# Optimization experiments

Measured on AMD Instinct MI355X. Metric: run time of the kernel, lower is better.

Reference implementation:

```python
import jax, jax.numpy as jnp
import numpy as np

B, S, D = 4, 1024, 1024      # batch, seq, dim
H = 1024                     # moe_inter_dim
E = 16                       # n_routed_experts
K = 2                        # n_activated_experts (top-k)
N_IN = 2                     # experts that consume x instead of embeddings
NSH = 2                      # n_shared_experts


def setup_inputs() -> dict:
    key = jax.random.key(0)
    ks = jax.random.split(key, 10)
    s = 0.02
    return {
        "embeddings": jax.random.normal(ks[0], (B, S, D), dtype=jnp.float32),
        "x": jax.random.normal(ks[1], (B * S, D), dtype=jnp.float32),
        "gate_w": jax.random.normal(ks[2], (E, D), dtype=jnp.float32) * s,
        "W1": jax.random.normal(ks[3], (E, D, H), dtype=jnp.float32) * s,
        "B1": jnp.zeros((E, H), dtype=jnp.float32),
        "W2": jax.random.normal(ks[4], (E, H, D), dtype=jnp.float32) * s,
        "B2": jnp.zeros((E, D), dtype=jnp.float32),
        "W3": jax.random.normal(ks[5], (E, D, H), dtype=jnp.float32) * s,
        "B3": jnp.zeros((E, H), dtype=jnp.float32),
        "sW1": jax.random.normal(ks[6], (D, NSH * H), dtype=jnp.float32) * s,
        "sB1": jnp.zeros((NSH * H,), dtype=jnp.float32),
        "sW2": jax.random.normal(ks[7], (NSH * H, D), dtype=jnp.float32) * s,
        "sB2": jnp.zeros((D,), dtype=jnp.float32),
    }


def _experts(inp, W1, B1, W2, B2, W3, B3):
    # SwiGLU expert applied for a stack of experts: inp [T,D], W* [e,...]
    h = jax.nn.silu(jnp.einsum('td,edh->eth', inp, W1) + B1[:, None, :]) \
        * (jnp.einsum('td,edh->eth', inp, W3) + B3[:, None, :])
    return jnp.einsum('eth,ehd->etd', h, W2) + B2[:, None, :]


def reference(embeddings, x, gate_w, W1, B1, W2, B2, W3, B3, sW1, sB1, sW2, sB2):
    shape = embeddings.shape
    emb = embeddings.reshape(-1, D)                       # [T, D]
    # Gate: softmax scores in fp32; n_groups==1, bias is None -> no group masking
    scores = jax.nn.softmax((emb @ gate_w.T).astype(jnp.float32), axis=-1)  # [T, E]
    top_w, top_i = jax.lax.top_k(scores, K)               # weights == gathered original_scores
    weights = top_w.astype(emb.dtype)                     # route_scale = 1.0
    # Combine coefficient per (token, expert): sum of routing weights of slots hitting e
    c = jnp.einsum('tk,tke->te', weights,
                   jax.nn.one_hot(top_i, E, dtype=weights.dtype))  # [T, E]
    # First N_IN experts consume x; the rest consume the embeddings
    out_in = _experts(x, W1[:N_IN], B1[:N_IN], W2[:N_IN], B2[:N_IN], W3[:N_IN], B3[:N_IN])
    out_emb = _experts(emb, W1[N_IN:], B1[N_IN:], W2[N_IN:], B2[N_IN:], W3[N_IN:], B3[N_IN:])
    y = jnp.einsum('te,etd->td', c, jnp.concatenate([out_in, out_emb], axis=0))
    # Shared experts (applied to every token)
    z = jax.nn.silu(emb @ sW1 + sB1) @ sW2 + sB2
    return (y + z).reshape(shape)
```

## Files before the change

kernel.cpp:

```cpp
#include <hip/hip_runtime.h>

#define T_TOK 4096
#define DIM   1024
#define HID   1024
#define NEXP  16
#define HSH   2048
#define NIN   2
#define MT_MAX 80

typedef __attribute__((ext_vector_type(8))) short bf8_t;
typedef __attribute__((ext_vector_type(4))) float f4_t;

__device__ __forceinline__ ushort f2b(float f) {
  unsigned u = __float_as_uint(f);
  u = (u + 0x7FFFu + ((u >> 16) & 1u)) >> 16;
  return (ushort)u;
}

__device__ __forceinline__ int tp_off(int r, int c) {
  return r * 64 + ((((c >> 3) ^ (r & 7)) << 3) | (c & 7));
}
__device__ __forceinline__ size_t tp_idx(int row, int col, int KT) {
  return ((size_t)((row >> 7) * KT + (col >> 6)) << 13) + tp_off(row & 127, col & 63);
}

__device__ __forceinline__ void gl_lds16(const ushort* g, ushort* l) {
  __builtin_amdgcn_global_load_lds(
      (const __attribute__((address_space(1))) void*)g,
      (__attribute__((address_space(3))) void*)l, 16, 0, 0);
}

template<bool DUAL>
__device__ __forceinline__ void mfma_tp(
    const ushort* __restrict__ aT, const ushort* __restrict__ b1T,
    const ushort* __restrict__ b3T, int nkt,
    ushort* As, ushort* Bs1, ushort* Bs3,
    f4_t acc1[4][4], f4_t acc3[4][4], int tid)
{
  const int lane = tid & 63, w = tid >> 6;
  const int wm = w & 1, wn = w >> 1;
  const int quad = lane >> 4, lr = lane & 15;
  const int soff = w << 11;
  const int l8 = lane * 8;

  for (int kt = 0; kt < nkt; kt++) {
    const size_t tb = (size_t)kt << 13;
    const ushort* ga = aT + tb + soff + l8;
    const ushort* gb = b1T + tb + soff + l8;
    #pragma unroll
    for (int d = 0; d < 4; d++) {
      gl_lds16(ga + (d << 9), As  + soff + (d << 9));
      gl_lds16(gb + (d << 9), Bs1 + soff + (d << 9));
    }
    if (DUAL) {
      const ushort* gc = b3T + tb + soff + l8;
      #pragma unroll
      for (int d = 0; d < 4; d++)
        gl_lds16(gc + (d << 9), Bs3 + soff + (d << 9));
    }
    __syncthreads();
    #pragma unroll
    for (int half = 0; half < 2; half++) {
      const int ch = (half << 2) + quad;
      bf8_t af[4];
      #pragma unroll
      for (int mi = 0; mi < 4; mi++) {
        const int r = wm * 64 + mi * 16 + lr;
        af[mi] = *(const bf8_t*)&As[r * 64 + ((ch ^ (r & 7)) << 3)];
      }
      #pragma unroll
      for (int ni = 0; ni < 4; ni++) {
        const int n = wn * 64 + ni * 16 + lr;
        bf8_t b1 = *(const bf8_t*)&Bs1[n * 64 + ((ch ^ (n & 7)) << 3)];
        #pragma unroll
        for (int mi = 0; mi < 4; mi++)
          acc1[mi][ni] = __builtin_amdgcn_mfma_f32_16x16x32_bf16(af[mi], b1, acc1[mi][ni], 0, 0, 0);
        if (DUAL) {
          bf8_t b3 = *(const bf8_t*)&Bs3[n * 64 + ((ch ^ (n & 7)) << 3)];
          #pragma unroll
          for (int mi = 0; mi < 4; mi++)
            acc3[mi][ni] = __builtin_amdgcn_mfma_f32_16x16x32_bf16(af[mi], b3, acc3[mi][ni], 0, 0, 0);
        }
      }
    }
    __syncthreads();
  }
}

__device__ __forceinline__ void tr_chunk(const float* __restrict__ src,
                                         ushort* __restrict__ dst,
                                         int R, int C, int band, int c, int tid,
                                         ushort* ts)
{
  const int KT = R >> 6;
  const int k0 = band * 64;
  #pragma unroll
  for (int i = 0; i < 16; i++) {
    const int idx = i * 256 + tid;
    const int r = idx >> 6, c4 = idx & 63;
    const float4 v = *(const float4*)(src + (size_t)(k0 + r) * C + c * 256 + c4 * 4);
    ushort4 u;
    u.x = f2b(v.x); u.y = f2b(v.y); u.z = f2b(v.z); u.w = f2b(v.w);
    *(ushort4*)&ts[r * 264 + ((c4 ^ ((r >> 3) & 7)) << 2)] = u;
  }
  __syncthreads();
  #pragma unroll
  for (int s = 0; s < 8; s++) {
    const int idx = s * 256 + tid;
    const int n = idx >> 3, kc = idx & 7;
    ushort o[8];
    #pragma unroll
    for (int j = 0; j < 8; j++)
      o[j] = ts[(kc * 8 + j) * 264 + (((n >> 2) ^ kc) << 2) + (n & 3)];
    *(uint4*)&dst[tp_idx(c * 256 + n, k0 + kc * 8, KT)] = *(uint4*)o;
  }
}

#define PREP_BLOCKS 4864
__launch_bounds__(256, 4)
__global__ void prep(const float* __restrict__ emb, const float* __restrict__ x_,
                     const float* __restrict__ gw,
                     const float* __restrict__ W1, const float* __restrict__ W3,
                     const float* __restrict__ W2,
                     const float* __restrict__ sW1, const float* __restrict__ sW2,
                     ushort* __restrict__ etp, ushort* __restrict__ xtp,
                     ushort* __restrict__ w1tp, ushort* __restrict__ w3tp,
                     ushort* __restrict__ w2tp,
                     ushort* __restrict__ sw1tp, ushort* __restrict__ sw2tp,
                     int* __restrict__ eA, int* __restrict__ eB,
                     float* __restrict__ wA, float* __restrict__ wB)
{
  __shared__ ushort ts[64 * 264];
  const int b = blockIdx.x;
  const int t = threadIdx.x;

  if (b < 3328) {
    const float* src; ushort* dst; int R, C, band, chunk;
    if (b < 3072) {
      const int z = b >> 6, rem = b & 63;
      band = rem >> 2; chunk = rem & 3;
      const int e = z & 15;
      src = ((z < 16) ? W1 : (z < 32) ? W3 : W2) + ((size_t)e << 20);
      dst = ((z < 16) ? w1tp : (z < 32) ? w3tp : w2tp) + ((size_t)e << 20);
      R = 1024; C = 1024;
    } else if (b < 3200) {
      const int i = b - 3072; band = i >> 3; chunk = i & 7;
      src = sW1; dst = sw1tp; R = 1024; C = 2048;
    } else {
      const int i = b - 3200; band = i >> 2; chunk = i & 3;
      src = sW2; dst = sw2tp; R = 2048; C = 1024;
    }
    tr_chunk(src, dst, R, C, band, chunk, t, ts);
  } else if (b < 4352) {
    const int w = t >> 6, lane = t & 63;
    const int tok = (b - 3328) * 4 + w;
    const float* er = emb + (size_t)tok * DIM + lane * 4;
    const float4 a0 = *(const float4*)(er);
    const float4 a1 = *(const float4*)(er + 256);
    const float4 a2 = *(const float4*)(er + 512);
    const float4 a3 = *(const float4*)(er + 768);
    float pe[NEXP];
    #pragma unroll
    for (int e = 0; e < NEXP; e++) {
      const float* gr = gw + (size_t)e * DIM + lane * 4;
      const float4 g0 = *(const float4*)(gr);
      const float4 g1 = *(const float4*)(gr + 256);
      const float4 g2 = *(const float4*)(gr + 512);
      const float4 g3 = *(const float4*)(gr + 768);
      float p = a0.x * g0.x + a0.y * g0.y + a0.z * g0.z + a0.w * g0.w;
      p += a1.x * g1.x + a1.y * g1.y + a1.z * g1.z + a1.w * g1.w;
      p += a2.x * g2.x + a2.y * g2.y + a2.z * g2.z + a2.w * g2.w;
      p += a3.x * g3.x + a3.y * g3.y + a3.z * g3.z + a3.w * g3.w;
      pe[e] = p;
    }
    #pragma unroll
    for (int e = 0; e < NEXP; e++) {
      float v = pe[e];
      v += __shfl_xor(v, 1);  v += __shfl_xor(v, 2);
      v += __shfl_xor(v, 4);  v += __shfl_xor(v, 8);
      v += __shfl_xor(v, 16); v += __shfl_xor(v, 32);
      pe[e] = v;
    }
    if (lane == 0) {
      float m1 = pe[0];
      #pragma unroll
      for (int j = 1; j < NEXP; j++) m1 = fmaxf(m1, pe[j]);
      float sum = 0.f;
      #pragma unroll
      for (int j = 0; j < NEXP; j++) sum += __expf(pe[j] - m1);
      int i0 = 0; float b0 = pe[0];
      #pragma unroll
      for (int j = 1; j < NEXP; j++) if (pe[j] > b0) { b0 = pe[j]; i0 = j; }
      int i1 = -1; float b1 = -3.402823466e38f;
      #pragma unroll
      for (int j = 0; j < NEXP; j++) if (j != i0 && pe[j] > b1) { b1 = pe[j]; i1 = j; }
      const float inv = 1.0f / sum;
      eA[tok] = i0; wA[tok] = __expf(b0 - m1) * inv;
      eB[tok] = i1; wB[tok] = __expf(b1 - m1) * inv;
    }
  } else {
    const int NC = (T_TOK * DIM) / 8;
    const int c0 = (b - 4352) * 256 + t;
    for (int c = c0; c < 2 * NC; c += 512 * 256) {
      const bool isE = c < NC;
      const int g = (isE ? c : c - NC) << 3;
      const float* src = isE ? emb : x_;
      const float4 v0 = *(const float4*)(src + g);
      const float4 v1 = *(const float4*)(src + g + 4);
      ushort tt[8];
      tt[0] = f2b(v0.x); tt[1] = f2b(v0.y); tt[2] = f2b(v0.z); tt[3] = f2b(v0.w);
      tt[4] = f2b(v1.x); tt[5] = f2b(v1.y); tt[6] = f2b(v1.z); tt[7] = f2b(v1.w);
      const int row = g >> 10, col = g & 1023;
      ushort* dst = isE ? etp : xtp;
      *(uint4*)&dst[tp_idx(row, col, 16)] = *(uint4*)tt;
    }
  }
}

__global__ void build_lists(const int* __restrict__ eA, const int* __restrict__ eB,
                            const float* __restrict__ wA, const float* __restrict__ wB,
                            int* __restrict__ cnt, int* __restrict__ list,
                            float* __restrict__ wl)
{
  const int e = blockIdx.x;
  __shared__ int wsum[4];
  __shared__ int sbase;
  const int tid = threadIdx.x;
  const int lane = tid & 63, wv = tid >> 6;
  if (tid == 0) sbase = 0;
  __syncthreads();
  for (int r = 0; r < 16; r++) {
    const int tk = r * 256 + tid;
    const int a = eA[tk], bb = eB[tk];
    const bool m = (a == e) || (bb == e);
    const float w = (a == e) ? wA[tk] : wB[tk];
    const unsigned long long bal = __ballot(m);
    const int pw = __popcll(bal & ((1ULL << lane) - 1ULL));
    if (lane == 63) wsum[wv] = pw + (m ? 1 : 0);
    __syncthreads();
    int base = sbase;
    for (int k = 0; k < wv; k++) base += wsum[k];
    if (m) {
      const int pos = base + pw;
      list[e * T_TOK + pos] = tk;
      wl[e * T_TOK + pos] = w;
    }
    __syncthreads();
    if (tid == 0) sbase += wsum[0] + wsum[1] + wsum[2] + wsum[3];
    __syncthreads();
  }
  if (tid == 0) cnt[e] = sbase;
}

__global__ void scan_offs(const int* __restrict__ cnt, int* __restrict__ offp,
                          int* __restrict__ tbl)
{
  if (blockIdx.x == 0 && threadIdx.x == 0) {
    int a = 0, nm = 0;
    for (int e = 0; e < NEXP; e++) {
      offp[e] = a;
      const int c = (cnt[e] + 127) & ~127;
      for (int r = 0; r < c; r += 128) { tbl[2 * nm] = e; tbl[2 * nm + 1] = a + r; nm++; }
      a += c;
    }
    offp[NEXP] = a;
    offp[NEXP + 1] = nm;
  }
}

__global__ void gather_a(const ushort* __restrict__ etp, const ushort* __restrict__ xtp,
                         const int* __restrict__ cnt, const int* __restrict__ offp,
                         const int* __restrict__ tbl, const int* __restrict__ list,
                         ushort* __restrict__ ag)
{
  const int mt = blockIdx.x >> 3;
  if (mt >= offp[NEXP + 1]) return;
  const int sl = blockIdx.x & 7;
  const int e = tbl[2 * mt], row0 = tbl[2 * mt + 1];
  const int ce = cnt[e];
  const int s0 = row0 - offp[e];
  const ushort* src = (e < NIN) ? xtp : etp;
  const int tid = threadIdx.x;
  #pragma unroll
  for (int rep = 0; rep < 8; rep++) {
    const int lin = rep * 256 + tid;
    const int r = lin >> 4, c8 = (sl * 128) + ((lin & 15) << 3);
    const int s = s0 + r;
    uint4 v = make_uint4(0u, 0u, 0u, 0u);
    if (s < ce) {
      const int tok = list[e * T_TOK + s];
      v = *(const uint4*)&src[tp_idx(tok, c8, 16)];
    }
    *(uint4*)&ag[tp_idx(row0 + r, c8, 16)] = v;
  }
}

__launch_bounds__(256, 3)
__global__ void stage1(const ushort* __restrict__ ag, const ushort* __restrict__ etp,
                       const ushort* __restrict__ w1tp, const ushort* __restrict__ w3tp,
                       const ushort* __restrict__ sw1tp,
                       const float* __restrict__ B1, const float* __restrict__ B3,
                       const float* __restrict__ sB1,
                       const int* __restrict__ offp, const int* __restrict__ tbl,
                       ushort* __restrict__ h_tp, ushort* __restrict__ hs_tp)
{
  __shared__ ushort As[8192], Bs1[8192], Bs3[8192];
  const int tid = threadIdx.x;
  const int lane = tid & 63, w = tid >> 6;
  const int wm = w & 1, wn = w >> 1;
  const int quad = lane >> 4, lr = lane & 15;
  const int b = blockIdx.x;

  f4_t acc1[4][4], acc3[4][4];
  const f4_t fz = {0.f, 0.f, 0.f, 0.f};
  #pragma unroll
  for (int i = 0; i < 4; i++)
    #pragma unroll
    for (int j = 0; j < 4; j++) { acc1[i][j] = fz; acc3[i][j] = fz; }

  if (b < 512) {
    const int m0 = (b >> 4) << 7;
    const int n0 = (b & 15) << 7;
    const ushort* aT = etp + ((size_t)((m0 >> 7) * 16) << 13);
    const ushort* bT = sw1tp + ((size_t)((n0 >> 7) * 16) << 13);
    mfma_tp<false>(aT, bT, nullptr, 16, As, Bs1, Bs3, acc1, acc3, tid);
    #pragma unroll
    for (int mi = 0; mi < 4; mi++) {
      #pragma unroll
      for (int r = 0; r < 4; r++) {
        const int row = m0 + wm * 64 + mi * 16 + quad * 4 + r;
        #pragma unroll
        for (int ni = 0; ni < 4; ni++) {
          const int col = n0 + wn * 64 + ni * 16 + lr;
          const float v = acc1[mi][ni][r] + sB1[col];
          const float sg = 1.0f / (1.0f + __expf(-v));
          hs_tp[tp_idx(row, col, 32)] = f2b(v * sg);
        }
      }
    }
  } else {
    const int t = b - 512;
    const int mt = t >> 3;
    if (mt >= offp[NEXP + 1]) return;
    const int n0 = (t & 7) << 7;
    const int e = tbl[2 * mt], row0 = tbl[2 * mt + 1];
    const ushort* aT  = ag + ((size_t)((row0 >> 7) * 16) << 13);
    const ushort* b1T = w1tp + ((size_t)e << 20) + ((size_t)((n0 >> 7) * 16) << 13);
    const ushort* b3T = w3tp + ((size_t)e << 20) + ((size_t)((n0 >> 7) * 16) << 13);
    mfma_tp<true>(aT, b1T, b3T, 16, As, Bs1, Bs3, acc1, acc3, tid);
    #pragma unroll
    for (int mi = 0; mi < 4; mi++) {
      #pragma unroll
      for (int r = 0; r < 4; r++) {
        const int grow = row0 + wm * 64 + mi * 16 + quad * 4 + r;
        #pragma unroll
        for (int ni = 0; ni < 4; ni++) {
          const int col = n0 + wn * 64 + ni * 16 + lr;
          const float v1 = acc1[mi][ni][r] + B1[e * HID + col];
          const float v3 = acc3[mi][ni][r] + B3[e * HID + col];
          const float sg = 1.0f / (1.0f + __expf(-v1));
          h_tp[tp_idx(grow, col, 16)] = f2b(v1 * sg * v3);
        }
      }
    }
  }
}

__launch_bounds__(256, 4)
__global__ void stage2(const ushort* __restrict__ h_tp, const ushort* __restrict__ hs_tp,
                       const ushort* __restrict__ w2tp, const ushort* __restrict__ sw2tp,
                       const float* __restrict__ B2, const float* __restrict__ sB2,
                       const int* __restrict__ cnt, const int* __restrict__ offp,
                       const int* __restrict__ tbl, const int* __restrict__ list,
                       const float* __restrict__ wl, float* __restrict__ y)
{
  __shared__ ushort As[8192], Bs[8192];
  const int tid = threadIdx.x;
  const int lane = tid & 63, w = tid >> 6;
  const int wm = w & 1, wn = w >> 1;
  const int quad = lane >> 4, lr = lane & 15;
  const int b = blockIdx.x;

  f4_t acc[4][4];
  const f4_t fz = {0.f, 0.f, 0.f, 0.f};
  #pragma unroll
  for (int i = 0; i < 4; i++)
    #pragma unroll
    for (int j = 0; j < 4; j++) acc[i][j] = fz;

  if (b < 256) {
    const int m0 = (b >> 3) << 7;
    const int n0 = (b & 7) << 7;
    const ushort* aT = hs_tp + ((size_t)((m0 >> 7) * 32) << 13);
    const ushort* bT = sw2tp + ((size_t)((n0 >> 7) * 32) << 13);
    mfma_tp<false>(aT, bT, nullptr, 32, As, Bs, Bs, acc, acc, tid);
    #pragma unroll
    for (int mi = 0; mi < 4; mi++) {
      #pragma unroll
      for (int r = 0; r < 4; r++) {
        const int row = m0 + wm * 64 + mi * 16 + quad * 4 + r;
        float* yr = y + (size_t)row * DIM;
        #pragma unroll
        for (int ni = 0; ni < 4; ni++) {
          const int col = n0 + wn * 64 + ni * 16 + lr;
          atomicAdd(&yr[col], acc[mi][ni][r] + sB2[col]);
        }
      }
    }
  } else {
    const int t = b - 256;
    const int mt = t >> 3;
    if (mt >= offp[NEXP + 1]) return;
    const int n0 = (t & 7) << 7;
    const int e = tbl[2 * mt], row0 = tbl[2 * mt + 1];
    const int ce = cnt[e];
    const int s0 = row0 - offp[e];
    const ushort* aT = h_tp + ((size_t)((row0 >> 7) * 16) << 13);
    const ushort* bT = w2tp + ((size_t)e << 20) + ((size_t)((n0 >> 7) * 16) << 13);
    mfma_tp<false>(aT, bT, nullptr, 16, As, Bs, Bs, acc, acc, tid);
    #pragma unroll
    for (int mi = 0; mi < 4; mi++) {
      #pragma unroll
      for (int r = 0; r < 4; r++) {
        const int rowl = s0 + wm * 64 + mi * 16 + quad * 4 + r;
        if (rowl < ce) {
          const int tok = list[e * T_TOK + rowl];
          const float wgt = wl[e * T_TOK + rowl];
          float* yr = y + (size_t)tok * DIM;
          #pragma unroll
          for (int ni = 0; ni < 4; ni++) {
            const int col = n0 + wn * 64 + ni * 16 + lr;
            atomicAdd(&yr[col], wgt * (acc[mi][ni][r] + B2[e * DIM + col]));
          }
        }
      }
    }
  }
}

extern "C" void kernel_launch(void* const* d_in, const int* in_sizes, int n_in,
                              void* d_out, int out_size, void* d_ws, size_t ws_size,
                              hipStream_t stream)
{
  const float* emb = (const float*)d_in[0];
  const float* x   = (const float*)d_in[1];
  const float* gw  = (const float*)d_in[2];
  const float* W1  = (const float*)d_in[3];
  const float* B1  = (const float*)d_in[4];
  const float* W2  = (const float*)d_in[5];
  const float* B2  = (const float*)d_in[6];
  const float* W3  = (const float*)d_in[7];
  const float* B3  = (const float*)d_in[8];
  const float* sW1 = (const float*)d_in[9];
  const float* sB1 = (const float*)d_in[10];
  const float* sW2 = (const float*)d_in[11];
  const float* sB2 = (const float*)d_in[12];
  float* y = (float*)d_out;

  char* ws = (char*)d_ws;
  const size_t MB = 1024ULL * 1024ULL;
  ushort* xtp   = (ushort*)(ws + 0);
  ushort* etp   = (ushort*)(ws + 16 * MB);
  ushort* w1tp  = (ushort*)(ws + 24 * MB);
  ushort* w3tp  = (ushort*)(ws + 56 * MB);
  ushort* w2tp  = (ushort*)(ws + 88 * MB);
  ushort* sw1tp = (ushort*)(ws + 120 * MB);
  ushort* sw2tp = (ushort*)(ws + 124 * MB);
  ushort* ag    = (ushort*)(ws + 128 * MB);
  ushort* h_tp  = (ushort*)(ws + 148 * MB);
  ushort* hs_tp = (ushort*)(ws + 168 * MB);
  int*   cnt    = (int*)(ws + 184 * MB);
  int*   offp   = cnt + 16;
  int*   tbl    = offp + 18;
  int*   list   = (int*)(ws + 184 * MB + 1024);
  float* wl     = (float*)(ws + 184 * MB + 1024 + 262144);
  int*   eA     = (int*)(ws + 185 * MB);
  int*   eB     = eA + T_TOK;
  float* wA     = (float*)(eB + T_TOK);
  float* wB     = wA + T_TOK;

  hipMemsetAsync(y, 0, (size_t)T_TOK * DIM * sizeof(float), stream);
  prep<<<PREP_BLOCKS, 256, 0, stream>>>(emb, x, gw, W1, W3, W2, sW1, sW2,
                                        etp, xtp, w1tp, w3tp, w2tp,
                                        sw1tp, sw2tp, eA, eB, wA, wB);
  build_lists<<<NEXP, 256, 0, stream>>>(eA, eB, wA, wB, cnt, list, wl);
  scan_offs<<<1, 64, 0, stream>>>(cnt, offp, tbl);
  gather_a<<<MT_MAX * 8, 256, 0, stream>>>(etp, xtp, cnt, offp, tbl, list, ag);
  stage1<<<512 + MT_MAX * 8, 256, 0, stream>>>(ag, etp, w1tp, w3tp, sw1tp,
                                               B1, B3, sB1, offp, tbl, h_tp, hs_tp);
  stage2<<<256 + MT_MAX * 8, 256, 0, stream>>>(h_tp, hs_tp, w2tp, sw2tp, B2, sB2,
                                               cnt, offp, tbl, list, wl, y);
}
```

Measured before the change: 485.3 us.

## Double-buffer MFMA K-loop, fuse token gather into stage1 loads, drop LDS padding

Reworks the shared MFMA GEMM loop so each 64-wide K tile is staged as two 32-wide halves in ping-pong LDS buffers, letting the next half load while the current one computes, with a new XOR swizzle. The separate gather_a kernel and its intermediate buffer go away: stage1 now loads routed token rows straight from the transposed activation tiles through per-lane row pointers built from the token lists. The prep transpose drops its LDS row padding (264 to 256) and raises the occupancy hint. This saves a kernel launch and a round trip through global memory. In exchange it adds address arithmetic and scattered row loads, and out-of-range rows now repeat the last valid token instead of being zero-filled.

```diff
diff --git a/kernel.cpp b/kernel.cpp
--- a/kernel.cpp
+++ b/kernel.cpp
@@ -30,59 +30,69 @@
       (__attribute__((address_space(3))) void*)l, 16, 0, 0);
 }
 
+__device__ __forceinline__ int src_off(int sr, int rd, int cp, int h) {
+  const int cg = h * 4 + (cp ^ ((rd >> 1) & 3));
+  return sr * 64 + ((cg ^ (sr & 7)) << 3);
+}
+
 template<bool DUAL>
 __device__ __forceinline__ void mfma_tp(
-    const ushort* __restrict__ aT, const ushort* __restrict__ b1T,
-    const ushort* __restrict__ b3T, int nkt,
-    ushort* As, ushort* Bs1, ushort* Bs3,
+    const ushort* pA00, const ushort* pA01,
+    const ushort* pA10, const ushort* pA11,
+    const ushort* b1T, const ushort* b3T,
+    int oB00, int oB01, int oB10, int oB11,
+    int nkt, ushort* As, ushort* Bs1, ushort* Bs3,
     f4_t acc1[4][4], f4_t acc3[4][4], int tid)
 {
   const int lane = tid & 63, w = tid >> 6;
   const int wm = w & 1, wn = w >> 1;
   const int quad = lane >> 4, lr = lane & 15;
-  const int soff = w << 11;
-  const int l8 = lane * 8;
-
-  for (int kt = 0; kt < nkt; kt++) {
-    const size_t tb = (size_t)kt << 13;
-    const ushort* ga = aT + tb + soff + l8;
-    const ushort* gb = b1T + tb + soff + l8;
-    #pragma unroll
-    for (int d = 0; d < 4; d++) {
-      gl_lds16(ga + (d << 9), As  + soff + (d << 9));
-      gl_lds16(gb + (d << 9), Bs1 + soff + (d << 9));
-    }
+  const int dst0 = w * 1024 + lane * 8;
+
+  auto stage = [&](int koff, ushort* dA, ushort* dB1, ushort* dB3,
+                   const ushort* a0, const ushort* a1, int ob0, int ob1) {
+    gl_lds16(a0 + koff, dA + dst0);
+    gl_lds16(a1 + koff, dA + dst0 + 512);
+    gl_lds16(b1T + ob0 + koff, dB1 + dst0);
+    gl_lds16(b1T + ob1 + koff, dB1 + dst0 + 512);
     if (DUAL) {
-      const ushort* gc = b3T + tb + soff + l8;
-      #pragma unroll
-      for (int d = 0; d < 4; d++)
-        gl_lds16(gc + (d << 9), Bs3 + soff + (d << 9));
-    }
-    __syncthreads();
-    #pragma unroll
-    for (int half = 0; half < 2; half++) {
-      const int ch = (half << 2) + quad;
-      bf8_t af[4];
-      #pragma unroll
-      for (int mi = 0; mi < 4; mi++) {
-        const int r = wm * 64 + mi * 16 + lr;
-        af[mi] = *(const bf8_t*)&As[r * 64 + ((ch ^ (r & 7)) << 3)];
-      }
-      #pragma unroll
-      for (int ni = 0; ni < 4; ni++) {
-        const int n = wn * 64 + ni * 16 + lr;
-        bf8_t b1 = *(const bf8_t*)&Bs1[n * 64 + ((ch ^ (n & 7)) << 3)];
+      gl_lds16(b3T + ob0 + koff, dB3 + dst0);
+      gl_lds16(b3T + ob1 + koff, dB3 + dst0 + 512);
+    }
+  };
+  auto compute = [&](const ushort* A, const ushort* B1, const ushort* B3) {
+    bf8_t af[4];
+    #pragma unroll
+    for (int mi = 0; mi < 4; mi++) {
+      const int r = wm * 64 + mi * 16 + lr;
+      af[mi] = *(const bf8_t*)&A[r * 32 + ((quad ^ ((r >> 1) & 3)) << 3)];
+    }
+    #pragma unroll
+    for (int ni = 0; ni < 4; ni++) {
+      const int n = wn * 64 + ni * 16 + lr;
+      const bf8_t b1 = *(const bf8_t*)&B1[n * 32 + ((quad ^ ((n >> 1) & 3)) << 3)];
+      #pragma unroll
+      for (int mi = 0; mi < 4; mi++)
+        acc1[mi][ni] = __builtin_amdgcn_mfma_f32_16x16x32_bf16(af[mi], b1, acc1[mi][ni], 0, 0, 0);
+      if (DUAL) {
+        const bf8_t b3 = *(const bf8_t*)&B3[n * 32 + ((quad ^ ((n >> 1) & 3)) << 3)];
         #pragma unroll
         for (int mi = 0; mi < 4; mi++)
-          acc1[mi][ni] = __builtin_amdgcn_mfma_f32_16x16x32_bf16(af[mi], b1, acc1[mi][ni], 0, 0, 0);
-        if (DUAL) {
-          bf8_t b3 = *(const bf8_t*)&Bs3[n * 64 + ((ch ^ (n & 7)) << 3)];
-          #pragma unroll
-          for (int mi = 0; mi < 4; mi++)
-            acc3[mi][ni] = __builtin_amdgcn_mfma_f32_16x16x32_bf16(af[mi], b3, acc3[mi][ni], 0, 0, 0);
-        }
+          acc3[mi][ni] = __builtin_amdgcn_mfma_f32_16x16x32_bf16(af[mi], b3, acc3[mi][ni], 0, 0, 0);
       }
     }
+  };
+
+  stage(0, As, Bs1, Bs3, pA00, pA10, oB00, oB10);
+  __syncthreads();
+  for (int kt = 0; kt < nkt; kt++) {
+    const int ko = kt << 13;
+    stage(ko, As + 4096, Bs1 + 4096, Bs3 + 4096, pA01, pA11, oB01, oB11);
+    compute(As, Bs1, Bs3);
+    __syncthreads();
+    if (kt + 1 < nkt)
+      stage(ko + 8192, As, Bs1, Bs3, pA00, pA10, oB00, oB10);
+    compute(As + 4096, Bs1 + 4096, Bs3 + 4096);
     __syncthreads();
   }
 }
@@ -101,7 +111,7 @@
     const float4 v = *(const float4*)(src + (size_t)(k0 + r) * C + c * 256 + c4 * 4);
     ushort4 u;
     u.x = f2b(v.x); u.y = f2b(v.y); u.z = f2b(v.z); u.w = f2b(v.w);
-    *(ushort4*)&ts[r * 264 + ((c4 ^ ((r >> 3) & 7)) << 2)] = u;
+    *(ushort4*)&ts[r * 256 + ((c4 ^ ((r >> 3) & 7)) << 2)] = u;
   }
   __syncthreads();
   #pragma unroll
@@ -111,13 +121,13 @@
     ushort o[8];
     #pragma unroll
     for (int j = 0; j < 8; j++)
-      o[j] = ts[(kc * 8 + j) * 264 + (((n >> 2) ^ kc) << 2) + (n & 3)];
+      o[j] = ts[(kc * 8 + j) * 256 + (((n >> 2) ^ kc) << 2) + (n & 3)];
     *(uint4*)&dst[tp_idx(c * 256 + n, k0 + kc * 8, KT)] = *(uint4*)o;
   }
 }
 
 #define PREP_BLOCKS 4864
-__launch_bounds__(256, 4)
+__launch_bounds__(256, 5)
 __global__ void prep(const float* __restrict__ emb, const float* __restrict__ x_,
                      const float* __restrict__ gw,
                      const float* __restrict__ W1, const float* __restrict__ W3,
@@ -130,7 +140,7 @@
                      int* __restrict__ eA, int* __restrict__ eB,
                      float* __restrict__ wA, float* __restrict__ wB)
 {
-  __shared__ ushort ts[64 * 264];
+  __shared__ ushort ts[64 * 256];
   const int b = blockIdx.x;
   const int t = threadIdx.x;
 
@@ -268,40 +278,14 @@
   }
 }
 
-__global__ void gather_a(const ushort* __restrict__ etp, const ushort* __restrict__ xtp,
-                         const int* __restrict__ cnt, const int* __restrict__ offp,
-                         const int* __restrict__ tbl, const int* __restrict__ list,
-                         ushort* __restrict__ ag)
-{
-  const int mt = blockIdx.x >> 3;
-  if (mt >= offp[NEXP + 1]) return;
-  const int sl = blockIdx.x & 7;
-  const int e = tbl[2 * mt], row0 = tbl[2 * mt + 1];
-  const int ce = cnt[e];
-  const int s0 = row0 - offp[e];
-  const ushort* src = (e < NIN) ? xtp : etp;
-  const int tid = threadIdx.x;
-  #pragma unroll
-  for (int rep = 0; rep < 8; rep++) {
-    const int lin = rep * 256 + tid;
-    const int r = lin >> 4, c8 = (sl * 128) + ((lin & 15) << 3);
-    const int s = s0 + r;
-    uint4 v = make_uint4(0u, 0u, 0u, 0u);
-    if (s < ce) {
-      const int tok = list[e * T_TOK + s];
-      v = *(const uint4*)&src[tp_idx(tok, c8, 16)];
-    }
-    *(uint4*)&ag[tp_idx(row0 + r, c8, 16)] = v;
-  }
-}
-
 __launch_bounds__(256, 3)
-__global__ void stage1(const ushort* __restrict__ ag, const ushort* __restrict__ etp,
+__global__ void stage1(const ushort* __restrict__ etp, const ushort* __restrict__ xtp,
                        const ushort* __restrict__ w1tp, const ushort* __restrict__ w3tp,
                        const ushort* __restrict__ sw1tp,
                        const float* __restrict__ B1, const float* __restrict__ B3,
                        const float* __restrict__ sB1,
-                       const int* __restrict__ offp, const int* __restrict__ tbl,
+                       const int* __restrict__ cnt, const int* __restrict__ offp,
+                       const int* __restrict__ tbl, const int* __restrict__ list,
                        ushort* __restrict__ h_tp, ushort* __restrict__ hs_tp)
 {
   __shared__ ushort As[8192], Bs1[8192], Bs3[8192];
@@ -309,6 +293,7 @@
   const int lane = tid & 63, w = tid >> 6;
   const int wm = w & 1, wn = w >> 1;
   const int quad = lane >> 4, lr = lane & 15;
+  const int r0 = w * 32 + (lane >> 2), r1 = r0 + 16, cp = lane & 3;
   const int b = blockIdx.x;
 
   f4_t acc1[4][4], acc3[4][4];
@@ -317,13 +302,18 @@
   for (int i = 0; i < 4; i++)
     #pragma unroll
     for (int j = 0; j < 4; j++) { acc1[i][j] = fz; acc3[i][j] = fz; }
+
+  const int o00 = src_off(r0, r0, cp, 0), o01 = src_off(r0, r0, cp, 1);
+  const int o10 = src_off(r1, r1, cp, 0), o11 = src_off(r1, r1, cp, 1);
 
   if (b < 512) {
     const int m0 = (b >> 4) << 7;
     const int n0 = (b & 15) << 7;
     const ushort* aT = etp + ((size_t)((m0 >> 7) * 16) << 13);
     const ushort* bT = sw1tp + ((size_t)((n0 >> 7) * 16) << 13);
-    mfma_tp<false>(aT, bT, nullptr, 16, As, Bs1, Bs3, acc1, acc3, tid);
+    mfma_tp<false>(aT + o00, aT + o01, aT + o10, aT + o11,
+                   bT, nullptr, o00, o01, o10, o11,
+                   16, As, Bs1, Bs3, acc1, acc3, tid);
     #pragma unroll
     for (int mi = 0; mi < 4; mi++) {
       #pragma unroll
@@ -344,10 +334,22 @@
     if (mt >= offp[NEXP + 1]) return;
     const int n0 = (t & 7) << 7;
     const int e = tbl[2 * mt], row0 = tbl[2 * mt + 1];
-    const ushort* aT  = ag + ((size_t)((row0 >> 7) * 16) << 13);
+    const int ce = cnt[e];
+    const int s0 = row0 - offp[e];
+    const ushort* src = (e < NIN) ? xtp : etp;
+    int sa = s0 + r0; if (sa >= ce) sa = ce - 1;
+    int sb = s0 + r1; if (sb >= ce) sb = ce - 1;
+    const int tokA = list[e * T_TOK + sa];
+    const int tokB = list[e * T_TOK + sb];
+    const ushort* tA = src + ((size_t)((tokA >> 7) * 16) << 13);
+    const ushort* tB = src + ((size_t)((tokB >> 7) * 16) << 13);
+    const int ra = tokA & 127, rb = tokB & 127;
     const ushort* b1T = w1tp + ((size_t)e << 20) + ((size_t)((n0 >> 7) * 16) << 13);
     const ushort* b3T = w3tp + ((size_t)e << 20) + ((size_t)((n0 >> 7) * 16) << 13);
-    mfma_tp<true>(aT, b1T, b3T, 16, As, Bs1, Bs3, acc1, acc3, tid);
+    mfma_tp<true>(tA + src_off(ra, r0, cp, 0), tA + src_off(ra, r0, cp, 1),
+                  tB + src_off(rb, r1, cp, 0), tB + src_off(rb, r1, cp, 1),
+                  b1T, b3T, o00, o01, o10, o11,
+                  16, As, Bs1, Bs3, acc1, acc3, tid);
     #pragma unroll
     for (int mi = 0; mi < 4; mi++) {
       #pragma unroll
@@ -379,6 +381,7 @@
   const int lane = tid & 63, w = tid >> 6;
   const int wm = w & 1, wn = w >> 1;
   const int quad = lane >> 4, lr = lane & 15;
+  const int r0 = w * 32 + (lane >> 2), r1 = r0 + 16, cp = lane & 3;
   const int b = blockIdx.x;
 
   f4_t acc[4][4];
@@ -387,13 +390,18 @@
   for (int i = 0; i < 4; i++)
     #pragma unroll
     for (int j = 0; j < 4; j++) acc[i][j] = fz;
+
+  const int o00 = src_off(r0, r0, cp, 0), o01 = src_off(r0, r0, cp, 1);
+  const int o10 = src_off(r1, r1, cp, 0), o11 = src_off(r1, r1, cp, 1);
 
   if (b < 256) {
     const int m0 = (b >> 3) << 7;
     const int n0 = (b & 7) << 7;
     const ushort* aT = hs_tp + ((size_t)((m0 >> 7) * 32) << 13);
     const ushort* bT = sw2tp + ((size_t)((n0 >> 7) * 32) << 13);
-    mfma_tp<false>(aT, bT, nullptr, 32, As, Bs, Bs, acc, acc, tid);
+    mfma_tp<false>(aT + o00, aT + o01, aT + o10, aT + o11,
+                   bT, nullptr, o00, o01, o10, o11,
+                   32, As, Bs, Bs, acc, acc, tid);
     #pragma unroll
     for (int mi = 0; mi < 4; mi++) {
       #pragma unroll
@@ -417,7 +425,9 @@
     const int s0 = row0 - offp[e];
     const ushort* aT = h_tp + ((size_t)((row0 >> 7) * 16) << 13);
     const ushort* bT = w2tp + ((size_t)e << 20) + ((size_t)((n0 >> 7) * 16) << 13);
-    mfma_tp<false>(aT, bT, nullptr, 16, As, Bs, Bs, acc, acc, tid);
+    mfma_tp<false>(aT + o00, aT + o01, aT + o10, aT + o11,
+                   bT, nullptr, o00, o01, o10, o11,
+                   16, As, Bs, Bs, acc, acc, tid);
     #pragma unroll
     for (int mi = 0; mi < 4; mi++) {
       #pragma unroll
@@ -466,7 +476,6 @@
   ushort* w2tp  = (ushort*)(ws + 88 * MB);
   ushort* sw1tp = (ushort*)(ws + 120 * MB);
   ushort* sw2tp = (ushort*)(ws + 124 * MB);
-  ushort* ag    = (ushort*)(ws + 128 * MB);
   ushort* h_tp  = (ushort*)(ws + 148 * MB);
   ushort* hs_tp = (ushort*)(ws + 168 * MB);
   int*   cnt    = (int*)(ws + 184 * MB);
@@ -485,9 +494,9 @@
                                         sw1tp, sw2tp, eA, eB, wA, wB);
   build_lists<<<NEXP, 256, 0, stream>>>(eA, eB, wA, wB, cnt, list, wl);
   scan_offs<<<1, 64, 0, stream>>>(cnt, offp, tbl);
-  gather_a<<<MT_MAX * 8, 256, 0, stream>>>(etp, xtp, cnt, offp, tbl, list, ag);
-  stage1<<<512 + MT_MAX * 8, 256, 0, stream>>>(ag, etp, w1tp, w3tp, sw1tp,
-                                               B1, B3, sB1, offp, tbl, h_tp, hs_tp);
+  stage1<<<512 + MT_MAX * 8, 256, 0, stream>>>(etp, xtp, w1tp, w3tp, sw1tp,
+                                               B1, B3, sB1, cnt, offp, tbl, list,
+                                               h_tp, hs_tp);
   stage2<<<256 + MT_MAX * 8, 256, 0, stream>>>(h_tp, hs_tp, w2tp, sw2tp, B2, sB2,
                                                cnt, offp, tbl, list, wl, y);
 }
```

After: 524.0 us. 8.0% more time.
